# Performance work log

Hardware: AMD Instinct MI355X
Metric: run time of the kernel (lower is better)

## Reference

```python
import math
import jax, jax.numpy as jnp
import numpy as np

B, T, C, H = 2, 2048, 1024, 16
MAX_SEQ = 2048


def _make_pe(max_seq: int, dim: int, base: float = 10000.0) -> np.ndarray:
    pe = np.zeros((max_seq, dim), dtype=np.float32)
    position = np.arange(max_seq, dtype=np.float32)[:, None]
    div_term = np.exp(np.arange(0, dim, 2, dtype=np.float32) * (-math.log(base) / dim))
    pe[:, 0::2] = np.sin(position * div_term)
    pe[:, 1::2] = np.cos(position * div_term)
    return pe


def setup_inputs() -> dict:
    key = jax.random.key(0)
    k1, k2, k3 = jax.random.split(key, 3)
    x = jax.random.normal(k1, (B, T, C), dtype=jnp.float32)
    # torch Linear default init scale ~ 1/sqrt(fan_in)
    w_qkv = jax.random.normal(k2, (3 * C, C), dtype=jnp.float32) / math.sqrt(C)
    w_proj = jax.random.normal(k3, (C, C), dtype=jnp.float32) / math.sqrt(C)
    pe = jnp.asarray(_make_pe(MAX_SEQ, C))
    return {"x": x, "w_qkv": w_qkv, "w_proj": w_proj, "pe": pe}


def reference(x, w_qkv, w_proj, pe):
    b, t, c = x.shape
    h = H
    d = c // h
    # RoPE module adds sinusoidal PE under torch.no_grad() -> stop_gradient
    xp = jax.lax.stop_gradient(x + pe[None, :t, :])
    qkv = xp @ w_qkv.T  # [b, t, 3c]
    q, k, v = jnp.split(qkv, 3, axis=-1)
    q = q.reshape(b, t, h, d).transpose(0, 2, 1, 3)  # bhtd
    k = k.reshape(b, t, h, d).transpose(0, 2, 1, 3)
    v = v.reshape(b, t, h, d).transpose(0, 2, 1, 3)
    att = jnp.einsum("bhqd,bhkd->bhqk", q, k) * (1.0 / math.sqrt(d))
    causal = jnp.tril(jnp.ones((t, t), dtype=bool))  # [t, t]
    att = jnp.where(causal[None, None], att, -jnp.inf)
    att = jax.nn.softmax(att, axis=-1)
    y = jnp.einsum("bhqk,bhkd->bhqd", att, v)
    y = y.transpose(0, 2, 1, 3).reshape(b, t, c)
    return y @ w_proj.T
```

## Files before the change

kernel.cpp:

```cpp
#include <hip/hip_runtime.h>
#include <cstdint>

typedef __bf16 bf16x8 __attribute__((ext_vector_type(8)));
typedef __bf16 bf16x4 __attribute__((ext_vector_type(4)));
typedef float  f32x4  __attribute__((ext_vector_type(4)));

static constexpr int kB = 2, kT = 2048, kC = 1024, kH = 16, kD = 64;
static constexpr int kK = 1024;

__device__ __forceinline__ uint16_t f2bf(float f) {
  uint32_t u = __builtin_bit_cast(uint32_t, f);
  u += 0x7FFFu + ((u >> 16) & 1u);
  return (uint16_t)(u >> 16);
}

__device__ __forceinline__ void gl_lds16(const void* g, void* l) {
  __builtin_amdgcn_global_load_lds((__attribute__((address_space(1))) void*)(void*)g,
                                   (__attribute__((address_space(3))) void*)l, 16, 0, 0);
}

__global__ __launch_bounds__(256) void prep_xpe(const float* __restrict__ x,
                                                const float* __restrict__ pe,
                                                uint16_t* __restrict__ xp) {
  const int i = blockIdx.x * 256 + threadIdx.x;
  const float4 xv = ((const float4*)x)[i];
  const int c4 = i & (kC / 4 - 1);
  const int t = (i / (kC / 4)) & (kT - 1);
  const float4 pv = ((const float4*)pe)[t * (kC / 4) + c4];
  ushort4 o;
  o.x = f2bf(xv.x + pv.x);
  o.y = f2bf(xv.y + pv.y);
  o.z = f2bf(xv.z + pv.z);
  o.w = f2bf(xv.w + pv.w);
  ((ushort4*)xp)[i] = o;
}

__global__ __launch_bounds__(256) void cast_w(const float* __restrict__ w,
                                              uint16_t* __restrict__ o) {
  const int i = blockIdx.x * 256 + threadIdx.x;
  const float4 v = ((const float4*)w)[i];
  ushort4 u;
  u.x = f2bf(v.x); u.y = f2bf(v.y); u.z = f2bf(v.z); u.w = f2bf(v.w);
  ((ushort4*)o)[i] = u;
}

template <int EPI>
__global__ __launch_bounds__(256) void gemm_bt(const uint16_t* __restrict__ A,
                                               const uint16_t* __restrict__ W,
                                               uint16_t* __restrict__ qb,
                                               uint16_t* __restrict__ kb,
                                               uint16_t* __restrict__ vT,
                                               float* __restrict__ out) {
  __shared__ char lds[32768];
  const int lane = threadIdx.x & 63;
  const int wid = threadIdx.x >> 6;
  const int l15 = lane & 15, l4 = lane >> 4;
  const int wm = wid >> 1, wn = wid & 1;
  const int m0 = blockIdx.x * 128, n0 = blockIdx.y * 128;

  f32x4 acc[4][4] = {};

  for (int k0 = 0; k0 < kK; k0 += 64) {
#pragma unroll
    for (int j = 0; j < 4; ++j) {
      const int off = wid * 4096 + j * 1024 + lane * 16;
      const int row = off >> 7;
      const int colb = (off & 127) ^ ((row & 7) << 4);
      gl_lds16((const char*)A + ((size_t)(m0 + row) * kK + k0) * 2 + colb,
               lds + wid * 4096 + j * 1024);
      gl_lds16((const char*)W + ((size_t)(n0 + row) * kK + k0) * 2 + colb,
               lds + 16384 + wid * 4096 + j * 1024);
    }
    __syncthreads();
#pragma unroll
    for (int ks = 0; ks < 2; ++ks) {
      bf16x8 af[4], bf_[4];
#pragma unroll
      for (int mt = 0; mt < 4; ++mt) {
        const int r = wm * 64 + mt * 16 + l15;
        const int cb = (l4 * 16 + ks * 64) ^ ((r & 7) << 4);
        af[mt] = *(const bf16x8*)(lds + r * 128 + cb);
      }
#pragma unroll
      for (int nt = 0; nt < 4; ++nt) {
        const int r = wn * 64 + nt * 16 + l15;
        const int cb = (l4 * 16 + ks * 64) ^ ((r & 7) << 4);
        bf_[nt] = *(const bf16x8*)(lds + 16384 + r * 128 + cb);
      }
#pragma unroll
      for (int mt = 0; mt < 4; ++mt)
#pragma unroll
        for (int nt = 0; nt < 4; ++nt)
          acc[mt][nt] = __builtin_amdgcn_mfma_f32_16x16x32_bf16(af[mt], bf_[nt],
                                                                acc[mt][nt], 0, 0, 0);
    }
    __syncthreads();
  }

#pragma unroll
  for (int mt = 0; mt < 4; ++mt) {
#pragma unroll
    for (int nt = 0; nt < 4; ++nt) {
#pragma unroll
      for (int r = 0; r < 4; ++r) {
        const int m = m0 + wm * 64 + mt * 16 + l4 * 4 + r;
        const int n = n0 + wn * 64 + nt * 16 + l15;
        const float v = acc[mt][nt][r];
        if constexpr (EPI == 0) {
          const int b = m >> 11, t = m & (kT - 1);
          const int sec = n >> 10, nn = n & (kC - 1);
          const int h = nn >> 6, d = nn & 63;
          const size_t bh = (size_t)(b * kH + h);
          if (sec == 0)
            qb[(bh * kT + t) * kD + d] = f2bf(v);
          else if (sec == 1)
            kb[(bh * kT + t) * kD + d] = f2bf(v);
          else
            vT[(bh * kD + d) * kT + t] = f2bf(v);
        } else {
          out[(size_t)m * kC + n] = v;
        }
      }
    }
  }
}

__global__ __launch_bounds__(256, 4) void attn(const uint16_t* __restrict__ qb,
                                               const uint16_t* __restrict__ kb,
                                               const uint16_t* __restrict__ vT,
                                               uint16_t* __restrict__ y) {
  __shared__ __align__(1024) char lds[40960];
  const int lane = threadIdx.x & 63;
  const int wid = threadIdx.x >> 6;
  const int l15 = lane & 15, l4 = lane >> 4;
  const int bh = blockIdx.x;
  const int qt = (int)(gridDim.y - 1) - (int)blockIdx.y;
  const int q0 = qt * 64 + wid * 16;
  const size_t base = (size_t)bh * kT * kD;
  const uint16_t* Q = qb + base;
  const uint16_t* Kp = kb + base;
  const uint16_t* Vt = vT + base;
  char* P = lds + 32768 + wid * 2048;
  const int xr = (l15 & 7) << 4;

  bf16x8 qf[2];
#pragma unroll
  for (int ks = 0; ks < 2; ++ks) {
    bf16x8 t = *(const bf16x8*)(Q + (size_t)(q0 + l15) * kD + ks * 32 + l4 * 8);
#pragma unroll
    for (int i = 0; i < 8; ++i) t[i] = (__bf16)((float)t[i] * 0.1803368801f);
    qf[ks] = t;
  }

  float m_ = -1e30f, l_ = 0.f;
  f32x4 o[4];
#pragma unroll
  for (int nt = 0; nt < 4; ++nt) o[nt] = (f32x4){0.f, 0.f, 0.f, 0.f};

  const int nkt = qt + 1;

  auto STAGE = [&](int bi, int k0) {
#pragma unroll
    for (int c = 0; c < 2; ++c) {
      const int call = wid * 2 + c;
      const int row = call * 8 + (lane >> 3);
      const int colb = (((lane & 7) ^ ((lane >> 3) & 7)) << 4);
      gl_lds16((const char*)Kp + ((size_t)(k0 + row) * kD) * 2 + colb,
               lds + bi * 8192 + call * 1024);
      gl_lds16((const char*)Vt + ((size_t)row * kT + k0) * 2 + colb,
               lds + 16384 + bi * 8192 + call * 1024);
    }
  };

  int cur = 0;
  STAGE(0, 0);
  for (int kt = 0; kt < nkt; ++kt) {
    const int k0 = kt * 64;
    const bool hasnext = (kt + 1 < nkt);
    if (hasnext) STAGE(cur ^ 1, k0 + 64);
    if (hasnext)
      asm volatile("s_waitcnt vmcnt(4)" ::: "memory");
    else
      asm volatile("s_waitcnt vmcnt(0)" ::: "memory");
    __builtin_amdgcn_s_barrier();
    asm volatile("" ::: "memory");

    const char* Kb = lds + cur * 8192;
    const char* Vb = lds + 16384 + cur * 8192;

    f32x4 s[4] = {};
    __builtin_amdgcn_s_setprio(1);
#pragma unroll
    for (int ks = 0; ks < 2; ++ks)
#pragma unroll
      for (int nt = 0; nt < 4; ++nt) {
        const bf16x8 kf =
            *(const bf16x8*)(Kb + (nt * 16 + l15) * 128 + ((ks * 64 + l4 * 16) ^ xr));
        s[nt] = __builtin_amdgcn_mfma_f32_16x16x32_bf16(kf, qf[ks], s[nt], 0, 0, 0);
      }
    __builtin_amdgcn_s_setprio(0);

    if (kt == nkt - 1) {
      const int qq = q0 + l15;
#pragma unroll
      for (int nt = 0; nt < 4; ++nt)
#pragma unroll
        for (int r = 0; r < 4; ++r)
          if (k0 + nt * 16 + l4 * 4 + r > qq) s[nt][r] = -1e30f;
    }

    float pm = s[0][0];
#pragma unroll
    for (int nt = 0; nt < 4; ++nt)
#pragma unroll
      for (int r = 0; r < 4; ++r) pm = fmaxf(pm, s[nt][r]);
    if (!__all(pm <= m_ + 11.0f)) {
      float rm = fmaxf(pm, __shfl_xor(pm, 16));
      rm = fmaxf(rm, __shfl_xor(rm, 32));
      const float newm = fmaxf(m_, rm);
      const float sc = exp2f(m_ - newm);
      m_ = newm;
      l_ *= sc;
#pragma unroll
      for (int nt = 0; nt < 4; ++nt)
#pragma unroll
        for (int r = 0; r < 4; ++r) o[nt][r] *= sc;
    }
    float ps = 0.f;
#pragma unroll
    for (int nt = 0; nt < 4; ++nt)
#pragma unroll
      for (int r = 0; r < 4; ++r) {
        const float p = exp2f(s[nt][r] - m_);
        s[nt][r] = p;
        ps += p;
      }
    l_ += ps;

#pragma unroll
    for (int nt = 0; nt < 4; ++nt) {
      bf16x4 pk;
#pragma unroll
      for (int r = 0; r < 4; ++r) pk[r] = (__bf16)s[nt][r];
      *(bf16x4*)(P + l15 * 128 + ((nt * 32 + l4 * 8) ^ xr)) = pk;
    }
    asm volatile("s_waitcnt lgkmcnt(0)" ::: "memory");
    __builtin_amdgcn_sched_barrier(0);

    bf16x8 pf[2];
#pragma unroll
    for (int ks = 0; ks < 2; ++ks)
      pf[ks] = *(const bf16x8*)(P + l15 * 128 + ((ks * 64 + l4 * 16) ^ xr));
    __builtin_amdgcn_s_setprio(1);
#pragma unroll
    for (int ks = 0; ks < 2; ++ks)
#pragma unroll
      for (int nt = 0; nt < 4; ++nt) {
        const bf16x8 vf =
            *(const bf16x8*)(Vb + (nt * 16 + l15) * 128 + ((ks * 64 + l4 * 16) ^ xr));
        o[nt] = __builtin_amdgcn_mfma_f32_16x16x32_bf16(vf, pf[ks], o[nt], 0, 0, 0);
      }
    __builtin_amdgcn_s_setprio(0);

    __builtin_amdgcn_s_barrier();
    asm volatile("" ::: "memory");
    cur ^= 1;
  }

  l_ += __shfl_xor(l_, 16);
  l_ += __shfl_xor(l_, 32);
  const float inv = 1.0f / l_;
  const int b = bh >> 4, h = bh & 15;
  const int q = q0 + l15;
#pragma unroll
  for (int nt = 0; nt < 4; ++nt) {
    bf16x4 yv;
#pragma unroll
    for (int r = 0; r < 4; ++r) yv[r] = (__bf16)(o[nt][r] * inv);
    *(bf16x4*)(y + ((size_t)(b * kT + q)) * kC + h * kD + nt * 16 + l4 * 4) = yv;
  }
}

extern "C" void kernel_launch(void* const* d_in, const int* in_sizes, int n_in,
                              void* d_out, int out_size, void* d_ws, size_t ws_size,
                              hipStream_t stream) {
  const float* x = (const float*)d_in[0];
  const float* wqkv = (const float*)d_in[1];
  const float* wproj = (const float*)d_in[2];
  const float* pe = (const float*)d_in[3];

  char* ws = (char*)d_ws;
  uint16_t* xp = (uint16_t*)(ws);
  uint16_t* wq = (uint16_t*)(ws + (size_t)(8u << 20));
  uint16_t* wp = (uint16_t*)(ws + (size_t)(14u << 20));
  uint16_t* qbuf = (uint16_t*)(ws + (size_t)(16u << 20));
  uint16_t* kbuf = (uint16_t*)(ws + (size_t)(24u << 20));
  uint16_t* vTb = (uint16_t*)(ws + (size_t)(32u << 20));

  prep_xpe<<<dim3(kB * kT * kC / 4 / 256), 256, 0, stream>>>(x, pe, xp);
  cast_w<<<dim3(3 * kC * kC / 4 / 256), 256, 0, stream>>>(wqkv, wq);
  cast_w<<<dim3(kC * kC / 4 / 256), 256, 0, stream>>>(wproj, wp);

  gemm_bt<0><<<dim3(32, 24), 256, 0, stream>>>(xp, wq, qbuf, kbuf, vTb, nullptr);

  attn<<<dim3(kB * kH, kT / 64), 256, 0, stream>>>(qbuf, kbuf, vTb, xp);

  gemm_bt<1><<<dim3(32, 8), 256, 0, stream>>>(xp, wp, nullptr, nullptr, nullptr,
                                              (float*)d_out);
}
```

Before: 116.3 us.

## Stage QKV GEMM epilogue through LDS for vectorized stores and remap blocks per XCD

The QKV GEMM epilogue now writes the bf16 results into a padded, swizzled LDS tile and then writes Q/K rows and transposed V rows to global memory with 16-byte vector stores. Before, each lane stored scattered 2-byte values, and the strided V-transpose writes were especially costly. Block indices are also remapped so that neighbouring M tiles land on the same XCD, to improve L2 reuse of the weight tiles. The cost is a larger LDS allocation and an extra barrier. The remap assumes a grid of 32 M-tiles by a multiple of 8 blocks.

```diff
diff --git a/kernel.cpp b/kernel.cpp
--- a/kernel.cpp
+++ b/kernel.cpp
@@ -51,25 +51,28 @@
                                                uint16_t* __restrict__ kb,
                                                uint16_t* __restrict__ vT,
                                                float* __restrict__ out) {
-  __shared__ char lds[32768];
+  __shared__ __align__(1024) char lds[EPI == 0 ? 34816 : 32768];
   const int lane = threadIdx.x & 63;
   const int wid = threadIdx.x >> 6;
   const int l15 = lane & 15, l4 = lane >> 4;
   const int wm = wid >> 1, wn = wid & 1;
-  const int m0 = blockIdx.x * 128, n0 = blockIdx.y * 128;
+  const int orig = (int)(blockIdx.y * gridDim.x + blockIdx.x);
+  const int xcd = orig & 7, j = orig >> 3;
+  const int m0 = (xcd * 4 + (j & 3)) * 128;
+  const int n0 = (j >> 2) * 128;
 
   f32x4 acc[4][4] = {};
 
   for (int k0 = 0; k0 < kK; k0 += 64) {
 #pragma unroll
-    for (int j = 0; j < 4; ++j) {
-      const int off = wid * 4096 + j * 1024 + lane * 16;
+    for (int jj = 0; jj < 4; ++jj) {
+      const int off = wid * 4096 + jj * 1024 + lane * 16;
       const int row = off >> 7;
       const int colb = (off & 127) ^ ((row & 7) << 4);
       gl_lds16((const char*)A + ((size_t)(m0 + row) * kK + k0) * 2 + colb,
-               lds + wid * 4096 + j * 1024);
+               lds + wid * 4096 + jj * 1024);
       gl_lds16((const char*)W + ((size_t)(n0 + row) * kK + k0) * 2 + colb,
-               lds + 16384 + wid * 4096 + j * 1024);
+               lds + 16384 + wid * 4096 + jj * 1024);
     }
     __syncthreads();
 #pragma unroll
@@ -97,31 +100,71 @@
     __syncthreads();
   }
 
-#pragma unroll
-  for (int mt = 0; mt < 4; ++mt) {
-#pragma unroll
-    for (int nt = 0; nt < 4; ++nt) {
-#pragma unroll
-      for (int r = 0; r < 4; ++r) {
-        const int m = m0 + wm * 64 + mt * 16 + l4 * 4 + r;
-        const int n = n0 + wn * 64 + nt * 16 + l15;
-        const float v = acc[mt][nt][r];
-        if constexpr (EPI == 0) {
-          const int b = m >> 11, t = m & (kT - 1);
-          const int sec = n >> 10, nn = n & (kC - 1);
-          const int h = nn >> 6, d = nn & 63;
-          const size_t bh = (size_t)(b * kH + h);
-          if (sec == 0)
-            qb[(bh * kT + t) * kD + d] = f2bf(v);
-          else if (sec == 1)
-            kb[(bh * kT + t) * kD + d] = f2bf(v);
-          else
-            vT[(bh * kD + d) * kT + t] = f2bf(v);
-        } else {
-          out[(size_t)m * kC + n] = v;
+  if constexpr (EPI == 0) {
+    const int sec = n0 >> 10;
+    if (sec < 2) {
+#pragma unroll
+      for (int mt = 0; mt < 4; ++mt)
+#pragma unroll
+        for (int nt = 0; nt < 4; ++nt)
+#pragma unroll
+          for (int r = 0; r < 4; ++r) {
+            const int m = wm * 64 + mt * 16 + l4 * 4 + r;
+            const int n = wn * 64 + nt * 16 + l15;
+            *(uint16_t*)(lds + m * 272 + ((n * 2) ^ (((m >> 2) & 3) << 4))) =
+                f2bf(acc[mt][nt][r]);
+          }
+    } else {
+#pragma unroll
+      for (int mt = 0; mt < 4; ++mt)
+#pragma unroll
+        for (int nt = 0; nt < 4; ++nt)
+#pragma unroll
+          for (int r = 0; r < 4; ++r) {
+            const int m = wm * 64 + mt * 16 + l4 * 4 + r;
+            const int n = wn * 64 + nt * 16 + l15;
+            *(uint16_t*)(lds + n * 272 + m * 2) = f2bf(acc[mt][nt][r]);
+          }
+    }
+    __syncthreads();
+    const int tid = threadIdx.x;
+    const int b = m0 >> 11, tbase = m0 & (kT - 1);
+    if (sec < 2) {
+      uint16_t* dst = (sec == 0) ? qb : kb;
+#pragma unroll
+      for (int i = 0; i < 8; ++i) {
+        const int g = i * 256 + tid;
+        const int ml = g >> 4;
+        const int c8 = (g & 15) * 8;
+        const bf16x8 v =
+            *(const bf16x8*)(lds + ml * 272 + ((c8 * 2) ^ (((ml >> 2) & 3) << 4)));
+        const int nn = (n0 & (kC - 1)) + c8;
+        const int h = nn >> 6, d = nn & 63;
+        *(bf16x8*)(dst + ((size_t)((b * kH + h) * kT + tbase + ml)) * kD + d) = v;
+      }
+    } else {
+#pragma unroll
+      for (int i = 0; i < 8; ++i) {
+        const int g = i * 256 + tid;
+        const int dl = g >> 4;
+        const int m8 = (g & 15) * 8;
+        const bf16x8 v = *(const bf16x8*)(lds + dl * 272 + m8 * 2);
+        const int nn = (n0 & (kC - 1)) + dl;
+        const int h = nn >> 6, d = nn & 63;
+        *(bf16x8*)(vT + ((size_t)((b * kH + h) * kD + d)) * kT + tbase + m8) = v;
+      }
+    }
+  } else {
+#pragma unroll
+    for (int mt = 0; mt < 4; ++mt)
+#pragma unroll
+      for (int nt = 0; nt < 4; ++nt)
+#pragma unroll
+        for (int r = 0; r < 4; ++r) {
+          const int m = m0 + wm * 64 + mt * 16 + l4 * 4 + r;
+          const int n = n0 + wn * 64 + nt * 16 + l15;
+          out[(size_t)m * kC + n] = acc[mt][nt][r];
         }
-      }
-    }
   }
 }
 
```

Measured after the change: 119.9 us. 1.03x slower.
